# Kernel tuning notes

Measured on AMD Instinct MI355X. Metric: run time of the kernel, lower is better.

Reference implementation:

```python
import jax, jax.numpy as jnp
import numpy as np

DIM = 1024
H = 16
HD = DIM // H
SCALE = HD ** -0.5
LAMBDA_INIT = 0.1
EPS = 1e-6


def setup_inputs() -> dict:
    key0 = jax.random.key(0)
    ks = jax.random.split(key0, 12)
    B, Nq, Nk = 2, 1024, 2048
    w = 0.02
    inp = {
        "query": jax.random.normal(ks[0], (B, Nq, DIM), jnp.float32),
        "key": jax.random.normal(ks[1], (B, Nk, DIM), jnp.float32),
        "value": jax.random.normal(ks[2], (B, Nk, DIM), jnp.float32),
        "qpos": jax.random.randint(ks[3], (B, Nq), 0, Nq, jnp.int32),
        "kpos": jax.random.randint(ks[4], (B, Nk), 0, Nk, jnp.int32),
        "q1_w": jax.random.normal(ks[5], (DIM, DIM), jnp.float32) * w,
        "q2_w": jax.random.normal(ks[6], (DIM, DIM), jnp.float32) * w,
        "kv1_w": jax.random.normal(ks[7], (2 * DIM, DIM), jnp.float32) * w,
        "kv2_w": jax.random.normal(ks[8], (2 * DIM, DIM), jnp.float32) * w,
        "proj_w": jax.random.normal(ks[9], (DIM, DIM), jnp.float32) * w,
        "proj_b": jnp.zeros((DIM,), jnp.float32),
        "norm_w": jnp.ones((DIM,), jnp.float32),
        "lambda_1": jnp.ones((1, H, 1, 1), jnp.float32),
        # layer_idx=0, max_layer=12 -> scale = 1/12
        "lambda_2": jnp.full((1, H, 1, 1), 1.0 - LAMBDA_INIT * (1.0 / 12.0), jnp.float32),
    }
    return inp


def _split_heads(x, B, N):
    # [B, N, DIM] -> [B, H, N, HD]
    return x.reshape(B, N, H, HD).transpose(0, 2, 1, 3)


def reference(query, key, value, qpos, kpos, q1_w, q2_w, kv1_w, kv2_w,
              proj_w, proj_b, norm_w, lambda_1, lambda_2):
    B, Nq, C = query.shape
    Nk = key.shape[1]

    q1 = _split_heads(query @ q1_w.T, B, Nq)
    q2 = _split_heads(query @ q2_w.T, B, Nq)

    kv1 = (key @ kv1_w.T).reshape(B, Nk, 2, H, HD).transpose(2, 0, 3, 1, 4)
    k1, v1 = kv1[0], kv1[1]  # [B, H, Nk, HD]
    kv2 = (key @ kv2_w.T).reshape(B, Nk, 2, H, HD).transpose(2, 0, 3, 1, 4)
    k2 = kv2[0]

    attn1 = jax.nn.softmax(jnp.einsum('bhqd,bhkd->bhqk', q1, k1) * SCALE, axis=-1)
    attn2 = jax.nn.softmax(jnp.einsum('bhqd,bhkd->bhqk', q2, k2) * SCALE, axis=-1)

    lambda_full = lambda_1 - lambda_2 + LAMBDA_INIT  # [1, H, 1, 1]
    diff_attn = attn1 - lambda_full * attn2

    x = jnp.einsum('bhqk,bhkd->bhqd', diff_attn, v1)
    x = x.transpose(0, 2, 1, 3).reshape(B, Nq, C)

    # RMSNorm (computed in float32 like the original)
    xf = x.astype(jnp.float32)
    xf = xf * jax.lax.rsqrt(jnp.mean(xf * xf, axis=-1, keepdims=True) + EPS) * norm_w
    x = xf.astype(x.dtype)

    return x @ proj_w.T + proj_b
```

## Files before the change

kernel.cpp:

```cpp
#include <hip/hip_runtime.h>
#include <cstdint>

typedef unsigned short u16;
typedef __bf16 bf16x8 __attribute__((ext_vector_type(8)));
typedef float f32x4 __attribute__((ext_vector_type(4)));
typedef float f32x16 __attribute__((ext_vector_type(16)));
typedef uint32_t u32x4 __attribute__((ext_vector_type(4)));

#define SCALE_LOG2E (0.125f * 1.44269504088896340736f)

__device__ __forceinline__ u16 f2bf(float f) {
    uint32_t u = __builtin_bit_cast(uint32_t, f);
    u += 0x7fff + ((u >> 16) & 1);
    return (u16)(u >> 16);
}
__device__ __forceinline__ float bf2f(u16 u) {
    return __builtin_bit_cast(float, (uint32_t)u << 16);
}

__device__ __forceinline__ void gload_lds16(const void* g, void* l) {
    __builtin_amdgcn_global_load_lds(
        (__attribute__((address_space(1))) void*)g,
        (__attribute__((address_space(3))) void*)l, 16, 0, 0);
}

__global__ __launch_bounds__(256) void cvt_all(const float* __restrict__ s0,
                                               const float* __restrict__ s1,
                                               const float* __restrict__ s2,
                                               const float* __restrict__ s3,
                                               const float* __restrict__ s4,
                                               const float* __restrict__ s5,
                                               const float* __restrict__ s6,
                                               u16* __restrict__ d0, u16* __restrict__ d1,
                                               u16* __restrict__ d2, u16* __restrict__ d3,
                                               u16* __restrict__ d4) {
    int i = blockIdx.x * 256 + threadIdx.x;
    const float* src;
    u16* dst;
    int off;
    if (i < 524288)       { src = s0; dst = d0; off = i; }
    else if (i < 1572864) { src = s1; dst = d1; off = i - 524288; }
    else if (i < 1835008) { src = s2; dst = d2; off = i - 1572864; }
    else if (i < 2097152) { src = s3; dst = d2 + (size_t)1024 * 1024; off = i - 1835008; }
    else if (i < 2621440) { src = s4; dst = d3; off = i - 2097152; }
    else if (i < 2883584) { src = s5; dst = d3 + (size_t)2048 * 1024; off = i - 2621440; }
    else                  { src = s6; dst = d4; off = i - 2883584; }
    float4 v = ((const float4*)src)[off];
    ushort4 o;
    o.x = f2bf(v.x); o.y = f2bf(v.y); o.z = f2bf(v.z); o.w = f2bf(v.w);
    ((ushort4*)dst)[off] = o;
}

__global__ __launch_bounds__(256) void gemm_qkv(const u16* __restrict__ Wq,
                                                const u16* __restrict__ Xq,
                                                const u16* __restrict__ Wkv,
                                                const u16* __restrict__ Xk,
                                                u16* __restrict__ q1s, u16* __restrict__ q2s,
                                                u16* __restrict__ k1f, u16* __restrict__ v1f,
                                                u16* __restrict__ k2f) {
    __shared__ u16 As[2][128 * 32];
    __shared__ u16 Bs[2][128 * 32];
    const int K = 1024;
    const int bid = blockIdx.x;
    int mode, bm, bn;
    const u16 *A, *B;
    if (bid < 256) {
        mode = 0; bm = bid >> 4; bn = bid & 15; A = Wq; B = Xq;
    } else {
        int t = bid - 256;
        mode = 1; bm = t % 24; bn = t / 24; A = Wkv; B = Xk;
    }
    const int tid = threadIdx.x;
    const int l = tid & 63, w = tid >> 6;
    const int c = l & 15, g = l >> 4;
    const int wr = w >> 1, wc = w & 1;

    f32x4 acc[4][4];
#pragma unroll
    for (int i = 0; i < 4; i++)
#pragma unroll
        for (int j = 0; j < 4; j++) acc[i][j] = f32x4{0.f, 0.f, 0.f, 0.f};

    const u16* Abase = A + (size_t)(bm * 128) * K;
    const u16* Bbase = B + (size_t)(bn * 128) * K;
    const int r0 = 32 * w + (l >> 2);
    const int chsw = ((l & 3) ^ ((l >> 3) & 3)) * 8;
    const int gsw = 8 * (g ^ ((c >> 1) & 3));

    int cur = 0;
    gload_lds16(Abase + (size_t)r0 * K + chsw,        &As[0][32 * w * 32]);
    gload_lds16(Abase + (size_t)(r0 + 16) * K + chsw, &As[0][(32 * w + 16) * 32]);
    gload_lds16(Bbase + (size_t)r0 * K + chsw,        &Bs[0][32 * w * 32]);
    gload_lds16(Bbase + (size_t)(r0 + 16) * K + chsw, &Bs[0][(32 * w + 16) * 32]);
    __syncthreads();

    for (int t = 0; t < 32; ++t) {
        if (t < 31) {
            const int kb = (t + 1) * 32;
            gload_lds16(Abase + (size_t)r0 * K + kb + chsw,        &As[cur ^ 1][32 * w * 32]);
            gload_lds16(Abase + (size_t)(r0 + 16) * K + kb + chsw, &As[cur ^ 1][(32 * w + 16) * 32]);
            gload_lds16(Bbase + (size_t)r0 * K + kb + chsw,        &Bs[cur ^ 1][32 * w * 32]);
            gload_lds16(Bbase + (size_t)(r0 + 16) * K + kb + chsw, &Bs[cur ^ 1][(32 * w + 16) * 32]);
        }
        bf16x8 af[4], bfr[4];
#pragma unroll
        for (int mi = 0; mi < 4; mi++)
            af[mi] = *(const bf16x8*)&As[cur][(64 * wr + 16 * mi + c) * 32 + gsw];
#pragma unroll
        for (int ni = 0; ni < 4; ni++)
            bfr[ni] = *(const bf16x8*)&Bs[cur][(64 * wc + 16 * ni + c) * 32 + gsw];
#pragma unroll
        for (int mi = 0; mi < 4; mi++)
#pragma unroll
            for (int ni = 0; ni < 4; ni++)
                acc[mi][ni] = __builtin_amdgcn_mfma_f32_16x16x32_bf16(
                    af[mi], bfr[ni], acc[mi][ni], 0, 0, 0);
        __syncthreads();
        cur ^= 1;
    }

#pragma unroll
    for (int mi = 0; mi < 4; mi++) {
        const int m0 = bm * 128 + 64 * wr + 16 * mi + 4 * g;
#pragma unroll
        for (int ni = 0; ni < 4; ni++) {
            const int n = bn * 128 + 64 * wc + 16 * ni + c;
            f32x4 v = acc[mi][ni];
            if (mode == 0) {
                int half = m0 >> 10, feat = m0 & 1023;
                int h = feat >> 6, hd0 = feat & 63;
                int b = n >> 10, nq = n & 1023;
                int bh = b * 16 + h;
                u16* dst = half ? q2s : q1s;
                size_t idx = ((size_t)(bh * 32 + (nq >> 5)) * 4 + (hd0 >> 4)) * 512
                           + (((hd0 >> 3) & 1) * 32 + (nq & 31)) * 8 + (hd0 & 7);
                ushort4 o;
                o.x = f2bf(v[0] * SCALE_LOG2E); o.y = f2bf(v[1] * SCALE_LOG2E);
                o.z = f2bf(v[2] * SCALE_LOG2E); o.w = f2bf(v[3] * SCALE_LOG2E);
                *(ushort4*)(dst + idx) = o;
            } else {
                int b = n >> 11, nk = n & 2047;
                if (m0 < 1024) {
                    int h = m0 >> 6, hd0 = m0 & 63, bh = b * 16 + h;
                    size_t idx = ((size_t)(bh * 64 + (nk >> 5)) * 4 + (hd0 >> 4)) * 512
                               + (((hd0 >> 3) & 1) * 32 + (nk & 31)) * 8 + (hd0 & 7);
                    ushort4 o;
                    o.x = f2bf(v[0]); o.y = f2bf(v[1]); o.z = f2bf(v[2]); o.w = f2bf(v[3]);
                    *(ushort4*)(k1f + idx) = o;
                } else if (m0 < 2048) {
                    int feat = m0 - 1024, h = feat >> 6, hd0 = feat & 63, bh = b * 16 + h;
#pragma unroll
                    for (int j = 0; j < 4; j++) {
                        int hd = hd0 + j;
                        size_t idx = ((size_t)(bh * 128 + (nk >> 4)) * 2 + (hd >> 5)) * 512
                                   + (((nk >> 3) & 1) * 32 + (hd & 31)) * 8 + (nk & 7);
                        v1f[idx] = f2bf(v[j]);
                    }
                } else {
                    int feat = m0 - 2048, h = feat >> 6, hd0 = feat & 63, bh = b * 16 + h;
                    size_t idx = ((size_t)(bh * 64 + (nk >> 5)) * 4 + (hd0 >> 4)) * 512
                               + (((hd0 >> 3) & 1) * 32 + (nk & 31)) * 8 + (hd0 & 7);
                    ushort4 o;
                    o.x = f2bf(v[0]); o.y = f2bf(v[1]); o.z = f2bf(v[2]); o.w = f2bf(v[3]);
                    *(ushort4*)(k2f + idx) = o;
                }
            }
        }
    }
}

__global__ __launch_bounds__(256) void gemm_proj(const u16* __restrict__ A,
                                                 const u16* __restrict__ B,
                                                 float* __restrict__ fo,
                                                 const float* __restrict__ bias) {
    __shared__ u16 As[2][128 * 32];
    __shared__ u16 Bs[2][64 * 32];
    const int K = 1024;
    const int bm = blockIdx.x >> 4, bn = blockIdx.x & 15;
    const int tid = threadIdx.x;
    const int l = tid & 63, w = tid >> 6;
    const int c = l & 15, g = l >> 4;
    const int wr = w >> 1, wc = w & 1;

    f32x4 acc[4][2];
#pragma unroll
    for (int i = 0; i < 4; i++)
#pragma unroll
        for (int j = 0; j < 2; j++) acc[i][j] = f32x4{0.f, 0.f, 0.f, 0.f};

    const u16* Abase = A + (size_t)(bm * 128) * K;
    const u16* Bbase = B + (size_t)(bn * 64) * K;
    const int rA = 32 * w + (l >> 2);
    const int rB = 16 * w + (l >> 2);
    const int chsw = ((l & 3) ^ ((l >> 3) & 3)) * 8;
    const int gsw = 8 * (g ^ ((c >> 1) & 3));

    int cur = 0;
    gload_lds16(Abase + (size_t)rA * K + chsw,        &As[0][32 * w * 32]);
    gload_lds16(Abase + (size_t)(rA + 16) * K + chsw, &As[0][(32 * w + 16) * 32]);
    gload_lds16(Bbase + (size_t)rB * K + chsw,        &Bs[0][16 * w * 32]);
    __syncthreads();

    for (int t = 0; t < 32; ++t) {
        if (t < 31) {
            const int kb = (t + 1) * 32;
            gload_lds16(Abase + (size_t)rA * K + kb + chsw,        &As[cur ^ 1][32 * w * 32]);
            gload_lds16(Abase + (size_t)(rA + 16) * K + kb + chsw, &As[cur ^ 1][(32 * w + 16) * 32]);
            gload_lds16(Bbase + (size_t)rB * K + kb + chsw,        &Bs[cur ^ 1][16 * w * 32]);
        }
        bf16x8 af[4], bfr[2];
#pragma unroll
        for (int mi = 0; mi < 4; mi++)
            af[mi] = *(const bf16x8*)&As[cur][(64 * wr + 16 * mi + c) * 32 + gsw];
#pragma unroll
        for (int ni = 0; ni < 2; ni++)
            bfr[ni] = *(const bf16x8*)&Bs[cur][(32 * wc + 16 * ni + c) * 32 + gsw];
#pragma unroll
        for (int mi = 0; mi < 4; mi++)
#pragma unroll
            for (int ni = 0; ni < 2; ni++)
                acc[mi][ni] = __builtin_amdgcn_mfma_f32_16x16x32_bf16(
                    af[mi], bfr[ni], acc[mi][ni], 0, 0, 0);
        __syncthreads();
        cur ^= 1;
    }

#pragma unroll
    for (int mi = 0; mi < 4; mi++)
#pragma unroll
        for (int ni = 0; ni < 2; ni++)
#pragma unroll
            for (int j = 0; j < 4; j++) {
                int m = bm * 128 + 64 * wr + 16 * mi + 4 * g + j;
                int n = bn * 64 + 32 * wc + 16 * ni + c;
                fo[(size_t)m * 1024 + n] = acc[mi][ni][j] + bias[n];
            }
}

__global__ __launch_bounds__(256) void attn_kernel(const u16* __restrict__ q1s,
                                                   const u16* __restrict__ q2s,
                                                   const u16* __restrict__ k1fm,
                                                   const u16* __restrict__ k2fm,
                                                   const u16* __restrict__ v1fm,
                                                   u16* __restrict__ Opart,
                                                   float* __restrict__ Lpart) {
    __shared__ u16 kv[2][6144];
    const int tid = threadIdx.x;
    const int l = tid & 63, w = tid >> 6;
    const int c5 = l & 31, hf = l >> 5;
    const int bid = blockIdx.x;
    const int xcd = bid & 7, slot = bid >> 3;
    const int bh = xcd * 4 + (slot >> 5);
    const int r = slot & 31;
    const int qt = r >> 2, s = r & 3;
    const int b = bh >> 4, head = bh & 15;
    const int q0 = qt * 128 + w * 32;

    const u16* k1t = k1fm + (size_t)bh * 64 * 2048;
    const u16* k2t = k2fm + (size_t)bh * 64 * 2048;
    const u16* vt  = v1fm + (size_t)bh * 128 * 1024;
    const u16* bases[3] = {k1t, k2t, vt};

    auto stage = [&](int buf, int t32) {
#pragma unroll
        for (int j = 0; j < 3; j++) {
            int q = w * 3 + j;
            const u16* src = bases[q >> 2] + (size_t)t32 * 2048 + (q & 3) * 512 + l * 8;
            gload_lds16(src, &kv[buf][q * 512]);
        }
    };

    bf16x8 qB1[4], qB2[4];
    {
        const u16* p1 = q1s + ((size_t)(bh * 32 + (q0 >> 5)) * 4) * 512 + l * 8;
        const u16* p2 = q2s + ((size_t)(bh * 32 + (q0 >> 5)) * 4) * 512 + l * 8;
#pragma unroll
        for (int d = 0; d < 4; d++) {
            qB1[d] = *(const bf16x8*)(p1 + d * 512);
            qB2[d] = *(const bf16x8*)(p2 + d * 512);
        }
    }

    f32x16 O1[2], O2[2];
#pragma unroll
    for (int dh = 0; dh < 2; dh++)
#pragma unroll
        for (int i = 0; i < 16; i++) { O1[dh][i] = 0.f; O2[dh][i] = 0.f; }
    float la1 = 0.f, la2 = 0.f;

    stage(0, s * 16);
    __syncthreads();
    int cur = 0;

    for (int it = 0; it < 16; it++) {
        if (it < 15) stage(cur ^ 1, s * 16 + it + 1);

        const u16* bufp = &kv[cur][0];
        {
            bf16x8 kA[4];
#pragma unroll
            for (int d = 0; d < 4; d++)
                kA[d] = *(const bf16x8*)(bufp + d * 512 + l * 8);
            f32x16 S;
#pragma unroll
            for (int i = 0; i < 16; i++) S[i] = 0.f;
#pragma unroll
            for (int d = 0; d < 4; d++)
                S = __builtin_amdgcn_mfma_f32_32x32x16_bf16(kA[d], qB1[d], S, 0, 0, 0);
            uint32_t dpk[8];
#pragma unroll
            for (int i = 0; i < 8; i++) {
                float pa = __builtin_exp2f(S[2 * i]);
                float pb = __builtin_exp2f(S[2 * i + 1]);
                la1 += pa + pb;
                asm("v_cvt_pk_bf16_f32 %0, %1, %2" : "=v"(dpk[i]) : "v"(pa), "v"(pb));
            }
            uint32_t a0 = dpk[0], b0 = dpk[2], a1 = dpk[1], b1 = dpk[3];
            asm("v_permlane32_swap_b32 %0, %1" : "+v"(a0), "+v"(b0));
            asm("v_permlane32_swap_b32 %0, %1" : "+v"(a1), "+v"(b1));
            u32x4 t0 = {a0, a1, b0, b1};
            bf16x8 pf0 = __builtin_bit_cast(bf16x8, t0);
            uint32_t a2 = dpk[4], b2 = dpk[6], a3 = dpk[5], b3 = dpk[7];
            asm("v_permlane32_swap_b32 %0, %1" : "+v"(a2), "+v"(b2));
            asm("v_permlane32_swap_b32 %0, %1" : "+v"(a3), "+v"(b3));
            u32x4 t1 = {a2, a3, b2, b3};
            bf16x8 pf1 = __builtin_bit_cast(bf16x8, t1);
#pragma unroll
            for (int dh = 0; dh < 2; dh++) {
                bf16x8 v0 = *(const bf16x8*)(bufp + 4096 + dh * 512 + l * 8);
                bf16x8 v1 = *(const bf16x8*)(bufp + 4096 + (2 + dh) * 512 + l * 8);
                O1[dh] = __builtin_amdgcn_mfma_f32_32x32x16_bf16(pf0, v0, O1[dh], 0, 0, 0);
                O1[dh] = __builtin_amdgcn_mfma_f32_32x32x16_bf16(pf1, v1, O1[dh], 0, 0, 0);
            }
        }
        {
            bf16x8 kA[4];
#pragma unroll
            for (int d = 0; d < 4; d++)
                kA[d] = *(const bf16x8*)(bufp + 2048 + d * 512 + l * 8);
            f32x16 S;
#pragma unroll
            for (int i = 0; i < 16; i++) S[i] = 0.f;
#pragma unroll
            for (int d = 0; d < 4; d++)
                S = __builtin_amdgcn_mfma_f32_32x32x16_bf16(kA[d], qB2[d], S, 0, 0, 0);
            uint32_t dpk[8];
#pragma unroll
            for (int i = 0; i < 8; i++) {
                float pa = __builtin_exp2f(S[2 * i]);
                float pb = __builtin_exp2f(S[2 * i + 1]);
                la2 += pa + pb;
                asm("v_cvt_pk_bf16_f32 %0, %1, %2" : "=v"(dpk[i]) : "v"(pa), "v"(pb));
            }
            uint32_t a0 = dpk[0], b0 = dpk[2], a1 = dpk[1], b1 = dpk[3];
            asm("v_permlane32_swap_b32 %0, %1" : "+v"(a0), "+v"(b0));
            asm("v_permlane32_swap_b32 %0, %1" : "+v"(a1), "+v"(b1));
            u32x4 t0 = {a0, a1, b0, b1};
            bf16x8 pf0 = __builtin_bit_cast(bf16x8, t0);
            uint32_t a2 = dpk[4], b2 = dpk[6], a3 = dpk[5], b3 = dpk[7];
            asm("v_permlane32_swap_b32 %0, %1" : "+v"(a2), "+v"(b2));
            asm("v_permlane32_swap_b32 %0, %1" : "+v"(a3), "+v"(b3));
            u32x4 t1 = {a2, a3, b2, b3};
            bf16x8 pf1 = __builtin_bit_cast(bf16x8, t1);
#pragma unroll
            for (int dh = 0; dh < 2; dh++) {
                bf16x8 v0 = *(const bf16x8*)(bufp + 4096 + dh * 512 + l * 8);
                bf16x8 v1 = *(const bf16x8*)(bufp + 4096 + (2 + dh) * 512 + l * 8);
                O2[dh] = __builtin_amdgcn_mfma_f32_32x32x16_bf16(pf0, v0, O2[dh], 0, 0, 0);
                O2[dh] = __builtin_amdgcn_mfma_f32_32x32x16_bf16(pf1, v1, O2[dh], 0, 0, 0);
            }
        }
        __syncthreads();
        cur ^= 1;
    }

    la1 += __shfl_xor(la1, 32, 64);
    la2 += __shfl_xor(la2, 32, 64);

#pragma unroll
    for (int dh = 0; dh < 2; dh++)
#pragma unroll
        for (int rr = 0; rr < 16; rr++) {
            int qrow = (rr & 3) + 8 * (rr >> 2) + 4 * hf;
            size_t rowg = (size_t)b * 1024 + q0 + qrow;
            size_t col = head * 64 + dh * 32 + c5;
            Opart[((size_t)(s * 2 + 0) * 2048 + rowg) * 1024 + col] = f2bf(O1[dh][rr]);
            Opart[((size_t)(s * 2 + 1) * 2048 + rowg) * 1024 + col] = f2bf(O2[dh][rr]);
        }
    if (hf == 0) {
        size_t rowg = (size_t)b * 1024 + q0 + c5;
        Lpart[((size_t)(s * 2 + 0) * 2048 + rowg) * 16 + head] = la1;
        Lpart[((size_t)(s * 2 + 1) * 2048 + rowg) * 16 + head] = la2;
    }
}

__global__ __launch_bounds__(256) void combine_rms(const u16* __restrict__ Opart,
                                                   const float* __restrict__ Lpart,
                                                   const float* __restrict__ lam1,
                                                   const float* __restrict__ lam2,
                                                   const float* __restrict__ nw,
                                                   u16* __restrict__ xn) {
    const int row = blockIdx.x, t = threadIdx.x;
    const int h = t >> 4;
    float a1[4] = {0.f, 0.f, 0.f, 0.f}, a2[4] = {0.f, 0.f, 0.f, 0.f};
    float li1 = 0.f, li2 = 0.f;
#pragma unroll
    for (int s = 0; s < 4; s++) {
        ushort4 u1 = ((const ushort4*)(Opart + ((size_t)(s * 2 + 0) * 2048 + row) * 1024))[t];
        ushort4 u2 = ((const ushort4*)(Opart + ((size_t)(s * 2 + 1) * 2048 + row) * 1024))[t];
        a1[0] += bf2f(u1.x); a1[1] += bf2f(u1.y); a1[2] += bf2f(u1.z); a1[3] += bf2f(u1.w);
        a2[0] += bf2f(u2.x); a2[1] += bf2f(u2.y); a2[2] += bf2f(u2.z); a2[3] += bf2f(u2.w);
        li1 += Lpart[((size_t)(s * 2 + 0) * 2048 + row) * 16 + h];
        li2 += Lpart[((size_t)(s * 2 + 1) * 2048 + row) * 16 + h];
    }
    float lam = lam1[h] - lam2[h] + 0.1f;
    float i1 = 1.0f / li1, i2 = lam / li2;
    float x0 = a1[0] * i1 - a2[0] * i2;
    float x1 = a1[1] * i1 - a2[1] * i2;
    float x2 = a1[2] * i1 - a2[2] * i2;
    float x3 = a1[3] * i1 - a2[3] * i2;
    float ss = x0 * x0 + x1 * x1 + x2 * x2 + x3 * x3;
#pragma unroll
    for (int off = 1; off < 64; off <<= 1) ss += __shfl_xor(ss, off, 64);
    __shared__ float ws4[4];
    if ((t & 63) == 0) ws4[t >> 6] = ss;
    __syncthreads();
    float tot = ws4[0] + ws4[1] + ws4[2] + ws4[3];
    float rs = rsqrtf(tot * (1.0f / 1024.0f) + 1e-6f);
    float4 wv = ((const float4*)nw)[t];
    ushort4 o;
    o.x = f2bf(x0 * rs * wv.x);
    o.y = f2bf(x1 * rs * wv.y);
    o.z = f2bf(x2 * rs * wv.z);
    o.w = f2bf(x3 * rs * wv.w);
    ((ushort4*)(xn + (size_t)row * 1024))[t] = o;
}

extern "C" void kernel_launch(void* const* d_in, const int* in_sizes, int n_in,
                              void* d_out, int out_size, void* d_ws, size_t ws_size,
                              hipStream_t stream) {
    const float* query  = (const float*)d_in[0];
    const float* key    = (const float*)d_in[1];
    const float* q1_w   = (const float*)d_in[5];
    const float* q2_w   = (const float*)d_in[6];
    const float* kv1_w  = (const float*)d_in[7];
    const float* kv2_w  = (const float*)d_in[8];
    const float* proj_w = (const float*)d_in[9];
    const float* proj_b = (const float*)d_in[10];
    const float* norm_w = (const float*)d_in[11];
    const float* lam1   = (const float*)d_in[12];
    const float* lam2   = (const float*)d_in[13];
    float* out = (float*)d_out;

    char* ws = (char*)d_ws;
    size_t off = 0;
    auto alloc = [&](size_t bytes) {
        void* p = ws + off;
        off += (bytes + 255) & ~(size_t)255;
        return p;
    };
    u16* Xq   = (u16*)alloc((size_t)2048 * 1024 * 2);
    u16* Xk   = (u16*)alloc((size_t)4096 * 1024 * 2);
    u16* Wq   = (u16*)alloc((size_t)2048 * 1024 * 2);
    u16* Wkv  = (u16*)alloc((size_t)3072 * 1024 * 2);
    u16* Wp   = (u16*)alloc((size_t)1024 * 1024 * 2);
    u16* q1sb = (u16*)alloc((size_t)32 * 1024 * 64 * 2);
    u16* q2sb = (u16*)alloc((size_t)32 * 1024 * 64 * 2);
    u16* k1fb = (u16*)alloc((size_t)32 * 2048 * 64 * 2);
    u16* k2fb = (u16*)alloc((size_t)32 * 2048 * 64 * 2);
    u16* v1fb = (u16*)alloc((size_t)32 * 64 * 2048 * 2);
    u16* Opart = (u16*)alloc((size_t)8 * 2048 * 1024 * 2);
    float* Lpart = (float*)alloc((size_t)8 * 2048 * 16 * 4);
    u16* xn   = (u16*)alloc((size_t)2048 * 1024 * 2);

    cvt_all<<<12288, 256, 0, stream>>>(query, key, q1_w, q2_w, kv1_w, kv2_w, proj_w,
                                       Xq, Xk, Wq, Wkv, Wp);

    gemm_qkv<<<1024, 256, 0, stream>>>(Wq, Xq, Wkv, Xk, q1sb, q2sb, k1fb, v1fb, k2fb);

    attn_kernel<<<1024, 256, 0, stream>>>(q1sb, q2sb, k1fb, k2fb, v1fb, Opart, Lpart);

    combine_rms<<<2048, 256, 0, stream>>>(Opart, Lpart, lam1, lam2, norm_w, xn);

    gemm_proj<<<256, 256, 0, stream>>>(xn, Wp, out, proj_b);
}
```

Baseline: 262.8 us.

## Split attention waves across the two branches and remap GEMM blocks per XCD

The attention kernel now gives each wave a single branch: two waves compute the first softmax branch and two compute the second for 64 query rows. This halves per-wave accumulator registers and doubles the grid to 2048 blocks. K/V staging is shared between the branches within a block, but each block covers fewer queries, so total K/V staging traffic doubles. It also adds s_setprio around the MFMA phases, and remaps block IDs in both GEMMs so that consecutive tiles land on the same XCD for better L2 locality.

```diff
diff --git a/kernel.cpp b/kernel.cpp
--- a/kernel.cpp
+++ b/kernel.cpp
@@ -61,7 +61,8 @@
     __shared__ u16 As[2][128 * 32];
     __shared__ u16 Bs[2][128 * 32];
     const int K = 1024;
-    const int bid = blockIdx.x;
+    const int rawbid = blockIdx.x;
+    const int bid = (rawbid & 7) * 128 + (rawbid >> 3);
     int mode, bm, bn;
     const u16 *A, *B;
     if (bid < 256) {
@@ -176,7 +177,9 @@
     __shared__ u16 As[2][128 * 32];
     __shared__ u16 Bs[2][64 * 32];
     const int K = 1024;
-    const int bm = blockIdx.x >> 4, bn = blockIdx.x & 15;
+    const int rawbid = blockIdx.x;
+    const int bid = (rawbid & 7) * 32 + (rawbid >> 3);
+    const int bm = bid >> 4, bn = bid & 15;
     const int tid = threadIdx.x;
     const int l = tid & 63, w = tid >> 6;
     const int c = l & 15, g = l >> 4;
@@ -250,11 +253,12 @@
     const int c5 = l & 31, hf = l >> 5;
     const int bid = blockIdx.x;
     const int xcd = bid & 7, slot = bid >> 3;
-    const int bh = xcd * 4 + (slot >> 5);
-    const int r = slot & 31;
+    const int bh = xcd * 4 + (slot >> 6);
+    const int r = slot & 63;
     const int qt = r >> 2, s = r & 3;
     const int b = bh >> 4, head = bh & 15;
-    const int q0 = qt * 128 + w * 32;
+    const int at = w >> 1;
+    const int q0 = qt * 64 + (w & 1) * 32;
 
     const u16* k1t = k1fm + (size_t)bh * 64 * 2048;
     const u16* k2t = k2fm + (size_t)bh * 64 * 2048;
@@ -270,113 +274,79 @@
         }
     };
 
-    bf16x8 qB1[4], qB2[4];
+    const u16* qs = at ? q2s : q1s;
+    bf16x8 qB[4];
     {
-        const u16* p1 = q1s + ((size_t)(bh * 32 + (q0 >> 5)) * 4) * 512 + l * 8;
-        const u16* p2 = q2s + ((size_t)(bh * 32 + (q0 >> 5)) * 4) * 512 + l * 8;
-#pragma unroll
-        for (int d = 0; d < 4; d++) {
-            qB1[d] = *(const bf16x8*)(p1 + d * 512);
-            qB2[d] = *(const bf16x8*)(p2 + d * 512);
-        }
-    }
-
-    f32x16 O1[2], O2[2];
+        const u16* p = qs + ((size_t)(bh * 32 + (q0 >> 5)) * 4) * 512 + l * 8;
+#pragma unroll
+        for (int d = 0; d < 4; d++) qB[d] = *(const bf16x8*)(p + d * 512);
+    }
+
+    f32x16 O[2];
 #pragma unroll
     for (int dh = 0; dh < 2; dh++)
 #pragma unroll
-        for (int i = 0; i < 16; i++) { O1[dh][i] = 0.f; O2[dh][i] = 0.f; }
-    float la1 = 0.f, la2 = 0.f;
+        for (int i = 0; i < 16; i++) O[dh][i] = 0.f;
+    float la = 0.f;
 
     stage(0, s * 16);
     __syncthreads();
     int cur = 0;
+    const int kofs = at * 2048;
 
     for (int it = 0; it < 16; it++) {
         if (it < 15) stage(cur ^ 1, s * 16 + it + 1);
 
         const u16* bufp = &kv[cur][0];
-        {
-            bf16x8 kA[4];
-#pragma unroll
-            for (int d = 0; d < 4; d++)
-                kA[d] = *(const bf16x8*)(bufp + d * 512 + l * 8);
-            f32x16 S;
-#pragma unroll
-            for (int i = 0; i < 16; i++) S[i] = 0.f;
-#pragma unroll
-            for (int d = 0; d < 4; d++)
-                S = __builtin_amdgcn_mfma_f32_32x32x16_bf16(kA[d], qB1[d], S, 0, 0, 0);
-            uint32_t dpk[8];
-#pragma unroll
-            for (int i = 0; i < 8; i++) {
-                float pa = __builtin_exp2f(S[2 * i]);
-                float pb = __builtin_exp2f(S[2 * i + 1]);
-                la1 += pa + pb;
-                asm("v_cvt_pk_bf16_f32 %0, %1, %2" : "=v"(dpk[i]) : "v"(pa), "v"(pb));
-            }
-            uint32_t a0 = dpk[0], b0 = dpk[2], a1 = dpk[1], b1 = dpk[3];
-            asm("v_permlane32_swap_b32 %0, %1" : "+v"(a0), "+v"(b0));
-            asm("v_permlane32_swap_b32 %0, %1" : "+v"(a1), "+v"(b1));
-            u32x4 t0 = {a0, a1, b0, b1};
-            bf16x8 pf0 = __builtin_bit_cast(bf16x8, t0);
-            uint32_t a2 = dpk[4], b2 = dpk[6], a3 = dpk[5], b3 = dpk[7];
-            asm("v_permlane32_swap_b32 %0, %1" : "+v"(a2), "+v"(b2));
-            asm("v_permlane32_swap_b32 %0, %1" : "+v"(a3), "+v"(b3));
-            u32x4 t1 = {a2, a3, b2, b3};
-            bf16x8 pf1 = __builtin_bit_cast(bf16x8, t1);
-#pragma unroll
-            for (int dh = 0; dh < 2; dh++) {
-                bf16x8 v0 = *(const bf16x8*)(bufp + 4096 + dh * 512 + l * 8);
-                bf16x8 v1 = *(const bf16x8*)(bufp + 4096 + (2 + dh) * 512 + l * 8);
-                O1[dh] = __builtin_amdgcn_mfma_f32_32x32x16_bf16(pf0, v0, O1[dh], 0, 0, 0);
-                O1[dh] = __builtin_amdgcn_mfma_f32_32x32x16_bf16(pf1, v1, O1[dh], 0, 0, 0);
-            }
-        }
-        {
-            bf16x8 kA[4];
-#pragma unroll
-            for (int d = 0; d < 4; d++)
-                kA[d] = *(const bf16x8*)(bufp + 2048 + d * 512 + l * 8);
-            f32x16 S;
-#pragma unroll
-            for (int i = 0; i < 16; i++) S[i] = 0.f;
-#pragma unroll
-            for (int d = 0; d < 4; d++)
-                S = __builtin_amdgcn_mfma_f32_32x32x16_bf16(kA[d], qB2[d], S, 0, 0, 0);
-            uint32_t dpk[8];
-#pragma unroll
-            for (int i = 0; i < 8; i++) {
-                float pa = __builtin_exp2f(S[2 * i]);
-                float pb = __builtin_exp2f(S[2 * i + 1]);
-                la2 += pa + pb;
-                asm("v_cvt_pk_bf16_f32 %0, %1, %2" : "=v"(dpk[i]) : "v"(pa), "v"(pb));
-            }
-            uint32_t a0 = dpk[0], b0 = dpk[2], a1 = dpk[1], b1 = dpk[3];
-            asm("v_permlane32_swap_b32 %0, %1" : "+v"(a0), "+v"(b0));
-            asm("v_permlane32_swap_b32 %0, %1" : "+v"(a1), "+v"(b1));
-            u32x4 t0 = {a0, a1, b0, b1};
-            bf16x8 pf0 = __builtin_bit_cast(bf16x8, t0);
-            uint32_t a2 = dpk[4], b2 = dpk[6], a3 = dpk[5], b3 = dpk[7];
-            asm("v_permlane32_swap_b32 %0, %1" : "+v"(a2), "+v"(b2));
-            asm("v_permlane32_swap_b32 %0, %1" : "+v"(a3), "+v"(b3));
-            u32x4 t1 = {a2, a3, b2, b3};
-            bf16x8 pf1 = __builtin_bit_cast(bf16x8, t1);
-#pragma unroll
-            for (int dh = 0; dh < 2; dh++) {
-                bf16x8 v0 = *(const bf16x8*)(bufp + 4096 + dh * 512 + l * 8);
-                bf16x8 v1 = *(const bf16x8*)(bufp + 4096 + (2 + dh) * 512 + l * 8);
-                O2[dh] = __builtin_amdgcn_mfma_f32_32x32x16_bf16(pf0, v0, O2[dh], 0, 0, 0);
-                O2[dh] = __builtin_amdgcn_mfma_f32_32x32x16_bf16(pf1, v1, O2[dh], 0, 0, 0);
-            }
-        }
+        bf16x8 kA[4];
+#pragma unroll
+        for (int d = 0; d < 4; d++)
+            kA[d] = *(const bf16x8*)(bufp + kofs + d * 512 + l * 8);
+
+        f32x16 S;
+#pragma unroll
+        for (int i = 0; i < 16; i++) S[i] = 0.f;
+        __builtin_amdgcn_s_setprio(1);
+#pragma unroll
+        for (int d = 0; d < 4; d++)
+            S = __builtin_amdgcn_mfma_f32_32x32x16_bf16(kA[d], qB[d], S, 0, 0, 0);
+        __builtin_amdgcn_s_setprio(0);
+
+        uint32_t dpk[8];
+#pragma unroll
+        for (int i = 0; i < 8; i++) {
+            float pa = __builtin_exp2f(S[2 * i]);
+            float pb = __builtin_exp2f(S[2 * i + 1]);
+            la += pa + pb;
+            asm("v_cvt_pk_bf16_f32 %0, %1, %2" : "=v"(dpk[i]) : "v"(pa), "v"(pb));
+        }
+        uint32_t a0 = dpk[0], b0 = dpk[2], a1 = dpk[1], b1 = dpk[3];
+        asm("v_permlane32_swap_b32 %0, %1" : "+v"(a0), "+v"(b0));
+        asm("v_permlane32_swap_b32 %0, %1" : "+v"(a1), "+v"(b1));
+        u32x4 t0 = {a0, a1, b0, b1};
+        bf16x8 pf0 = __builtin_bit_cast(bf16x8, t0);
+        uint32_t a2 = dpk[4], b2 = dpk[6], a3 = dpk[5], b3 = dpk[7];
+        asm("v_permlane32_swap_b32 %0, %1" : "+v"(a2), "+v"(b2));
+        asm("v_permlane32_swap_b32 %0, %1" : "+v"(a3), "+v"(b3));
+        u32x4 t1 = {a2, a3, b2, b3};
+        bf16x8 pf1 = __builtin_bit_cast(bf16x8, t1);
+
+        __builtin_amdgcn_s_setprio(1);
+#pragma unroll
+        for (int dh = 0; dh < 2; dh++) {
+            bf16x8 v0 = *(const bf16x8*)(bufp + 4096 + dh * 512 + l * 8);
+            bf16x8 v1 = *(const bf16x8*)(bufp + 4096 + (2 + dh) * 512 + l * 8);
+            O[dh] = __builtin_amdgcn_mfma_f32_32x32x16_bf16(pf0, v0, O[dh], 0, 0, 0);
+            O[dh] = __builtin_amdgcn_mfma_f32_32x32x16_bf16(pf1, v1, O[dh], 0, 0, 0);
+        }
+        __builtin_amdgcn_s_setprio(0);
         __syncthreads();
         cur ^= 1;
     }
 
-    la1 += __shfl_xor(la1, 32, 64);
-    la2 += __shfl_xor(la2, 32, 64);
-
+    la += __shfl_xor(la, 32, 64);
+
+    const int plane = s * 2 + at;
 #pragma unroll
     for (int dh = 0; dh < 2; dh++)
 #pragma unroll
@@ -384,13 +354,11 @@
             int qrow = (rr & 3) + 8 * (rr >> 2) + 4 * hf;
             size_t rowg = (size_t)b * 1024 + q0 + qrow;
             size_t col = head * 64 + dh * 32 + c5;
-            Opart[((size_t)(s * 2 + 0) * 2048 + rowg) * 1024 + col] = f2bf(O1[dh][rr]);
-            Opart[((size_t)(s * 2 + 1) * 2048 + rowg) * 1024 + col] = f2bf(O2[dh][rr]);
+            Opart[((size_t)plane * 2048 + rowg) * 1024 + col] = f2bf(O[dh][rr]);
         }
     if (hf == 0) {
         size_t rowg = (size_t)b * 1024 + q0 + c5;
-        Lpart[((size_t)(s * 2 + 0) * 2048 + rowg) * 16 + head] = la1;
-        Lpart[((size_t)(s * 2 + 1) * 2048 + rowg) * 16 + head] = la2;
+        Lpart[((size_t)plane * 2048 + rowg) * 16 + head] = la;
     }
 }
 
@@ -478,7 +446,7 @@
 
     gemm_qkv<<<1024, 256, 0, stream>>>(Wq, Xq, Wkv, Xk, q1sb, q2sb, k1fb, v1fb, k2fb);
 
-    attn_kernel<<<1024, 256, 0, stream>>>(q1sb, q2sb, k1fb, k2fb, v1fb, Opart, Lpart);
+    attn_kernel<<<2048, 256, 0, stream>>>(q1sb, q2sb, k1fb, k2fb, v1fb, Opart, Lpart);
 
     combine_rms<<<2048, 256, 0, stream>>>(Opart, Lpart, lam1, lam2, norm_w, xn);
 
```

Measured after the change: 264.9 us. About the same (+0.8%).
